# Performance work log

Hardware: AMD Instinct MI355X
Metric: run time of the kernel (lower is better)

## Reference

```python
import jax, jax.numpy as jnp
import numpy as np

N_RES = 8192
N_IN = 128
BATCH = 16
RES_NNZ = int(0.1 * N_RES * N_RES)  # 6710886
IN_NNZ = int(0.1 * N_RES * N_IN)    # 104857
LEAK = 0.9


def spmm_coo(vals, rows, cols, inputs, n_out):
    """COO SpMM: out[b, r] = sum_{n: rows[n]==r} vals[n] * inputs[b, cols[n]].
    Equivalent to (coo_matmat(vals, rows, cols, inputs.T, shape=(n_out, F)).T)."""
    contrib = vals[:, None] * inputs.T[cols]  # [nnz, B]
    return jax.ops.segment_sum(contrib, rows, num_segments=n_out).T  # [B, n_out]


def leaky_erf(z, state, a=LEAK):
    return (1.0 - a) * state + a * jax.scipy.special.erf(z)


def setup_inputs() -> dict:
    key = jax.random.key(0)
    ks = jax.random.split(key, 10)
    return {
        "state": jax.random.normal(ks[0], (BATCH, N_RES), jnp.float32),
        "x": jax.random.normal(ks[1], (BATCH, N_IN), jnp.float32),
        "res_vals": jax.random.normal(ks[2], (RES_NNZ,), jnp.float32),
        "res_rows": jax.random.randint(ks[3], (RES_NNZ,), 0, N_RES, jnp.int32),
        "res_cols": jax.random.randint(ks[4], (RES_NNZ,), 0, N_RES, jnp.int32),
        "res_bias": jax.random.normal(ks[5], (N_RES,), jnp.float32),
        "in_vals": jax.random.normal(ks[6], (IN_NNZ,), jnp.float32),
        "in_rows": jax.random.randint(ks[7], (IN_NNZ,), 0, N_RES, jnp.int32),
        "in_cols": jax.random.randint(ks[8], (IN_NNZ,), 0, N_IN, jnp.int32),
        "in_bias": jax.random.normal(ks[9], (N_RES,), jnp.float32),
    }


def reference(state, x, res_vals, res_rows, res_cols, res_bias,
              in_vals, in_rows, in_cols, in_bias):
    z_res = spmm_coo(res_vals, res_rows, res_cols, state, N_RES) + res_bias
    z_in = spmm_coo(in_vals, in_rows, in_cols, x, N_RES) + in_bias
    return leaky_erf(z_in + z_res, state)
```

## Files before the change

kernel.cpp:

```cpp
#include <hip/hip_runtime.h>
#include <math.h>

#define N_RES 8192
#define N_IN  128
#define BATCH 16
#define LEAK  0.9f

#define NBK    128
#define CAP1B  55296
#define CHUNK1 4096
#define CHUNK2 4096
#define SB2    14
#define TBLK   128


#define OFF_SRCT 0
#define OFF_BCUR (1u << 20)
#define OFF_Z    (2u << 20)
#define OFF_E1   (8u << 20)
#define REQ_A    ((size_t)OFF_E1 + (size_t)NBK * CAP1B * 8)

__global__ __launch_bounds__(256, 4) void pass1_fused(
    const float* __restrict__ state,
    const float* __restrict__ x,
    const float* __restrict__ vres, const int* __restrict__ rres,
    const int* __restrict__ cres, int nres, int nbres,
    const float* __restrict__ vin, const int* __restrict__ rin,
    const int* __restrict__ cin, int nin, int nchunks,
    float* __restrict__ srcT,
    float* __restrict__ z,
    uint2* __restrict__ e1,
    int* __restrict__ bcur) {
  int tid = threadIdx.x;

  if (blockIdx.x >= nchunks) {
    int idx0 = (blockIdx.x - nchunks) * 256 + tid;
    const int stride = TBLK * 256;
    for (int i = idx0; i < N_RES * BATCH; i += stride) {
      int b = i >> 13;
      int r = i & (N_RES - 1);
      srcT[r * BATCH + b] = state[i];
      z[i] = 0.0f;
    }
    for (int i = idx0; i < N_IN * BATCH; i += stride) {
      int b = i >> 7;
      int c = i & (N_IN - 1);
      srcT[(N_RES + c) * BATCH + b] = x[i];
    }
    return;
  }

  const float* vals; const int* rows; const int* cols;
  int nnz, col_off, base;
  if (blockIdx.x < nbres) {
    vals = vres; rows = rres; cols = cres; nnz = nres; col_off = 0;
    base = blockIdx.x * CHUNK1;
  } else {
    vals = vin; rows = rin; cols = cin; nnz = nin; col_off = N_RES;
    base = (blockIdx.x - nbres) * CHUNK1;
  }

  __shared__ uint2 stg[CHUNK1];
  __shared__ int hist[NBK];
  __shared__ int lbase[NBK];
  __shared__ int gbase[NBK];
  __shared__ int wsum[2];
  int wave = tid >> 6, lane = tid & 63;

  if (tid < NBK) hist[tid] = 0;
  __syncthreads();

  int n = nnz - base;
  if (n > CHUNK1) n = CHUNK1;

  uint2 ent[16];
  int lp[16];
  unsigned msk = 0;
#pragma unroll
  for (int g = 0; g < 4; ++g) {
    int i0 = (g * 256 + tid) * 4;
    if (i0 + 3 < n) {
      int4 r4 = *(const int4*)(rows + base + i0);
      int4 c4 = *(const int4*)(cols + base + i0);
      float4 v4 = *(const float4*)(vals + base + i0);
      int rr_[4] = {r4.x, r4.y, r4.z, r4.w};
      int cc_[4] = {c4.x, c4.y, c4.z, c4.w};
      float vv_[4] = {v4.x, v4.y, v4.z, v4.w};
#pragma unroll
      for (int j = 0; j < 4; ++j) {
        int e = g * 4 + j;
        ent[e] = make_uint2(__float_as_uint(vv_[j]),
                            ((unsigned)rr_[j] << 14) |
                                (unsigned)(cc_[j] + col_off));
        msk |= 1u << e;
        lp[e] = atomicAdd(&hist[rr_[j] >> 6], 1);
      }
    } else {
#pragma unroll
      for (int j = 0; j < 4; ++j) {
        int e = g * 4 + j, i = i0 + j;
        if (i < n) {
          int r = rows[base + i];
          int c = cols[base + i] + col_off;
          float v = vals[base + i];
          ent[e] = make_uint2(__float_as_uint(v),
                              ((unsigned)r << 14) | (unsigned)c);
          msk |= 1u << e;
          lp[e] = atomicAdd(&hist[r >> 6], 1);
        }
      }
    }
  }
  __syncthreads();

  int h = 0, v = 0;
  if (tid < NBK) {
    h = hist[tid];
    v = h;
#pragma unroll
    for (int d = 1; d < 64; d <<= 1) {
      int t = __shfl_up(v, d);
      if (lane >= d) v += t;
    }
    if (lane == 63) wsum[wave] = v;
  }
  __syncthreads();
  if (tid < NBK) {
    int off = (wave == 1) ? wsum[0] : 0;
    lbase[tid] = off + v - h;
    gbase[tid] = h ? atomicAdd(&bcur[tid], h) : 0;
  }
  __syncthreads();
#pragma unroll
  for (int e = 0; e < 16; ++e) {
    if (msk & (1u << e)) {
      int b = (int)(ent[e].y >> 20);
      stg[lbase[b] + lp[e]] = ent[e];
    }
  }
  __syncthreads();
  for (int i = tid; i < n; i += 256) {
    uint2 ld = stg[i];
    int b = (int)(ld.y >> 20);
    int p = gbase[b] + (i - lbase[b]);
    if (p < CAP1B) e1[(size_t)b * CAP1B + p] = ld;
  }
}

__global__ __launch_bounds__(512, 8) void pass2_accum(
    const uint2* __restrict__ e1,
    const int* __restrict__ bcur,
    const float* __restrict__ srcT,
    float* __restrict__ z) {
  int bucket = blockIdx.y;
  int ch = blockIdx.x;
  int tid = threadIdx.x;

  int cnt = bcur[bucket];
  if (cnt > CAP1B) cnt = CAP1B;
  int base = ch * CHUNK2;
  if (base >= cnt) return;
  int n = cnt - base;
  if (n > CHUNK2) n = CHUNK2;

  __shared__ uint2 stg[CHUNK2];
  __shared__ int hist[64];
  __shared__ int sbase[65];
  int wave = tid >> 6, lane = tid & 63;
  if (tid < 64) hist[tid] = 0;
  __syncthreads();

  const uint2* __restrict__ src = e1 + (size_t)bucket * CAP1B + base;
  uint2 ent[8];
  int lp[8];
  unsigned msk = 0;
#pragma unroll
  for (int g = 0; g < 4; ++g) {
    int i = (g * 512 + tid) * 2;
    int e = g * 2;
    if (i + 1 < n) {
      uint4 q = *(const uint4*)(src + i);
      ent[e]     = make_uint2(q.x, q.y);
      ent[e + 1] = make_uint2(q.z, q.w);
      msk |= 3u << e;
      lp[e]     = atomicAdd(&hist[(ent[e].y >> 14) & 63u], 1);
      lp[e + 1] = atomicAdd(&hist[(ent[e + 1].y >> 14) & 63u], 1);
    } else if (i < n) {
      ent[e] = src[i];
      msk |= 1u << e;
      lp[e] = atomicAdd(&hist[(ent[e].y >> 14) & 63u], 1);
    }
  }
  __syncthreads();
  if (tid < 64) {
    int hh = hist[tid];
    int vv = hh;
#pragma unroll
    for (int d = 1; d < 64; d <<= 1) {
      int t = __shfl_up(vv, d);
      if (lane >= d) vv += t;
    }
    sbase[tid] = vv - hh;
    if (tid == 63) sbase[64] = vv;
  }
  __syncthreads();
#pragma unroll
  for (int e = 0; e < 8; ++e)
    if (msk & (1u << e))
      stg[sbase[(ent[e].y >> 14) & 63u] + lp[e]] = ent[e];
  __syncthreads();

  int eoff = lane >> 2;
  int bq = lane & 3;
  const float4* __restrict__ s4 = (const float4*)srcT;

  for (int rr = wave * 8; rr < wave * 8 + 8; ++rr) {
    int s0 = sbase[rr], s1 = sbase[rr + 1];
    float4 acc = make_float4(0.f, 0.f, 0.f, 0.f);
    int i0 = s0;
    for (; i0 + 32 <= s1; i0 += 32) {
      uint2 eA = stg[i0 + eoff];
      uint2 eB = stg[i0 + 16 + eoff];
      float4 sA = s4[(int)(eA.y & 16383u) * 4 + bq];
      float4 sB = s4[(int)(eB.y & 16383u) * 4 + bq];
      float vA = __uint_as_float(eA.x);
      float vB = __uint_as_float(eB.x);
      acc.x += vA * sA.x;
      acc.y += vA * sA.y;
      acc.z += vA * sA.z;
      acc.w += vA * sA.w;
      acc.x += vB * sB.x;
      acc.y += vB * sB.y;
      acc.z += vB * sB.z;
      acc.w += vB * sB.w;
    }
    if (i0 + 16 <= s1) {
      uint2 eA = stg[i0 + eoff];
      float4 sA = s4[(int)(eA.y & 16383u) * 4 + bq];
      float vA = __uint_as_float(eA.x);
      acc.x += vA * sA.x;
      acc.y += vA * sA.y;
      acc.z += vA * sA.z;
      acc.w += vA * sA.w;
      i0 += 16;
    }
    if (i0 < s1) {
      int e = i0 + eoff;
      if (e < s1) {
        uint2 eA = stg[e];
        float4 sA = s4[(int)(eA.y & 16383u) * 4 + bq];
        float vA = __uint_as_float(eA.x);
        acc.x += vA * sA.x;
        acc.y += vA * sA.y;
        acc.z += vA * sA.z;
        acc.w += vA * sA.w;
      }
    }
#pragma unroll
    for (int m = 4; m <= 32; m <<= 1) {
      acc.x += __shfl_xor(acc.x, m);
      acc.y += __shfl_xor(acc.y, m);
      acc.z += __shfl_xor(acc.z, m);
      acc.w += __shfl_xor(acc.w, m);
    }
    if (lane < 4) {
      float* zp = z + (size_t)(bucket * 64 + rr) * BATCH + lane * 4;
      unsafeAtomicAdd(zp + 0, acc.x);
      unsafeAtomicAdd(zp + 1, acc.y);
      unsafeAtomicAdd(zp + 2, acc.z);
      unsafeAtomicAdd(zp + 3, acc.w);
    }
  }
}

__global__ __launch_bounds__(256) void finalize_z(
    const float* __restrict__ z, const float* __restrict__ state,
    const float* __restrict__ res_bias, const float* __restrict__ in_bias,
    float* __restrict__ out) {
  int tid = blockIdx.x * 256 + threadIdx.x;
  if (tid >= BATCH * N_RES) return;
  int b = tid >> 13;
  int r = tid & (N_RES - 1);
  float zz = z[r * 16 + b] + res_bias[r] + in_bias[r];
  out[tid] = (1.0f - LEAK) * state[tid] + LEAK * erff(zz);
}

__global__ __launch_bounds__(256) void transpose_nb(
    const float* __restrict__ state, const float* __restrict__ x,
    float* __restrict__ srcT) {
  int tid = blockIdx.x * 256 + threadIdx.x;
  if (tid < N_RES * BATCH) {
    int b = tid >> 13;
    int r = tid & (N_RES - 1);
    srcT[r * BATCH + b] = state[tid];
  }
  if (tid < N_IN * BATCH) {
    int b = tid >> 7;
    int c = tid & (N_IN - 1);
    srcT[(N_RES + c) * BATCH + b] = x[tid];
  }
}

__global__ __launch_bounds__(256) void spmm_atomic(
    const float* __restrict__ vals, const int* __restrict__ rows,
    const int* __restrict__ cols, const float* __restrict__ srcT,
    int col_off, float* __restrict__ zz, int nnz) {
  int i = blockIdx.x * blockDim.x + threadIdx.x;
  if (i >= nnz) return;
  float v = vals[i];
  int r = rows[i];
  int c = cols[i] + col_off;
  const float4* __restrict__ sp = (const float4*)(srcT + c * BATCH);
  float* zr = zz + r * BATCH;
#pragma unroll
  for (int qq = 0; qq < 4; ++qq) {
    float4 s = sp[qq];
    unsafeAtomicAdd(zr + qq * 4 + 0, v * s.x);
    unsafeAtomicAdd(zr + qq * 4 + 1, v * s.y);
    unsafeAtomicAdd(zr + qq * 4 + 2, v * s.z);
    unsafeAtomicAdd(zr + qq * 4 + 3, v * s.w);
  }
}

extern "C" void kernel_launch(void* const* d_in, const int* in_sizes, int n_in,
                              void* d_out, int out_size, void* d_ws, size_t ws_size,
                              hipStream_t stream) {
  const float* state    = (const float*)d_in[0];
  const float* x        = (const float*)d_in[1];
  const float* res_vals = (const float*)d_in[2];
  const int*   res_rows = (const int*)d_in[3];
  const int*   res_cols = (const int*)d_in[4];
  const float* res_bias = (const float*)d_in[5];
  const float* in_vals  = (const float*)d_in[6];
  const int*   in_rows  = (const int*)d_in[7];
  const int*   in_cols  = (const int*)d_in[8];
  const float* in_bias  = (const float*)d_in[9];

  const int res_nnz = in_sizes[2];
  const int in_nnz  = in_sizes[6];

  char* ws = (char*)d_ws;
  float* srcT = (float*)(ws + OFF_SRCT);
  float* z    = (float*)(ws + OFF_Z);
  float* out = (float*)d_out;

  if (ws_size >= REQ_A) {
    int* bcur = (int*)(ws + OFF_BCUR);
    uint2* e1 = (uint2*)(ws + OFF_E1);
    int nbres = (res_nnz + CHUNK1 - 1) / CHUNK1;
    int nbin  = (in_nnz + CHUNK1 - 1) / CHUNK1;
    int nchunks = nbres + nbin;

    hipMemsetAsync(bcur, 0, NBK * sizeof(int), stream);

    pass1_fused<<<nchunks + TBLK, 256, 0, stream>>>(
        state, x, res_vals, res_rows, res_cols, res_nnz, nbres,
        in_vals, in_rows, in_cols, in_nnz, nchunks, srcT, z, e1, bcur);

    pass2_accum<<<dim3(SB2, NBK), 512, 0, stream>>>(e1, bcur, srcT, z);

    finalize_z<<<512, 256, 0, stream>>>(z, state, res_bias, in_bias, out);
  } else {
    hipMemsetAsync(z, 0, N_RES * BATCH * sizeof(float), stream);
    transpose_nb<<<512, 256, 0, stream>>>(state, x, srcT);
    spmm_atomic<<<(res_nnz + 255) / 256, 256, 0, stream>>>(
        res_vals, res_rows, res_cols, srcT, 0, z, res_nnz);
    spmm_atomic<<<(in_nnz + 255) / 256, 256, 0, stream>>>(
        in_vals, in_rows, in_cols, srcT, N_RES, z, in_nnz);
    finalize_z<<<512, 256, 0, stream>>>(z, state, res_bias, in_bias, out);
  }
}
```

Baseline: 212.4 us.

## Double pass1 chunk/block size and unroll pass2 gather loop with dual accumulators

Pass1 now runs 512-thread blocks that each bin an 8192-entry chunk, halving the block count and the global bucket atomics per entry. Pass2's inner gather loop is unrolled to four gathers per iteration into two accumulators, with a scheduling barrier so all loads issue before the FMAs, raising memory-level parallelism. The larger staging buffer raises LDS use per block and may lower occupancy. Code that still assumes 256 threads could misbehave.

```diff
diff --git a/kernel.cpp b/kernel.cpp
--- a/kernel.cpp
+++ b/kernel.cpp
@@ -8,7 +8,7 @@
 
 #define NBK    128
 #define CAP1B  55296
-#define CHUNK1 4096
+#define CHUNK1 8192
 #define CHUNK2 4096
 #define SB2    14
 #define TBLK   128
@@ -20,7 +20,7 @@
 #define OFF_E1   (8u << 20)
 #define REQ_A    ((size_t)OFF_E1 + (size_t)NBK * CAP1B * 8)
 
-__global__ __launch_bounds__(256, 4) void pass1_fused(
+__global__ __launch_bounds__(512, 4) void pass1_fused(
     const float* __restrict__ state,
     const float* __restrict__ x,
     const float* __restrict__ vres, const int* __restrict__ rres,
@@ -34,8 +34,8 @@
   int tid = threadIdx.x;
 
   if (blockIdx.x >= nchunks) {
-    int idx0 = (blockIdx.x - nchunks) * 256 + tid;
-    const int stride = TBLK * 256;
+    int idx0 = (blockIdx.x - nchunks) * 512 + tid;
+    const int stride = TBLK * 512;
     for (int i = idx0; i < N_RES * BATCH; i += stride) {
       int b = i >> 13;
       int r = i & (N_RES - 1);
@@ -78,7 +78,7 @@
   unsigned msk = 0;
 #pragma unroll
   for (int g = 0; g < 4; ++g) {
-    int i0 = (g * 256 + tid) * 4;
+    int i0 = (g * 512 + tid) * 4;
     if (i0 + 3 < n) {
       int4 r4 = *(const int4*)(rows + base + i0);
       int4 c4 = *(const int4*)(cols + base + i0);
@@ -139,7 +139,7 @@
     }
   }
   __syncthreads();
-  for (int i = tid; i < n; i += 256) {
+  for (int i = tid; i < n; i += 512) {
     uint2 ld = stg[i];
     int b = (int)(ld.y >> 20);
     int p = gbase[b] + (i - lbase[b]);
@@ -216,32 +216,52 @@
 
   for (int rr = wave * 8; rr < wave * 8 + 8; ++rr) {
     int s0 = sbase[rr], s1 = sbase[rr + 1];
-    float4 acc = make_float4(0.f, 0.f, 0.f, 0.f);
+    float4 accA = make_float4(0.f, 0.f, 0.f, 0.f);
+    float4 accB = make_float4(0.f, 0.f, 0.f, 0.f);
     int i0 = s0;
-    for (; i0 + 32 <= s1; i0 += 32) {
+    for (; i0 + 64 <= s1; i0 += 64) {
+      uint2 eA = stg[i0 + eoff];
+      uint2 eB = stg[i0 + 16 + eoff];
+      uint2 eC = stg[i0 + 32 + eoff];
+      uint2 eD = stg[i0 + 48 + eoff];
+      float4 sA = s4[(int)(eA.y & 16383u) * 4 + bq];
+      float4 sB = s4[(int)(eB.y & 16383u) * 4 + bq];
+      float4 sC = s4[(int)(eC.y & 16383u) * 4 + bq];
+      float4 sD = s4[(int)(eD.y & 16383u) * 4 + bq];
+      __builtin_amdgcn_sched_barrier(0);
+      float vA = __uint_as_float(eA.x);
+      float vB = __uint_as_float(eB.x);
+      float vC = __uint_as_float(eC.x);
+      float vD = __uint_as_float(eD.x);
+      accA.x += vA * sA.x; accA.y += vA * sA.y;
+      accA.z += vA * sA.z; accA.w += vA * sA.w;
+      accB.x += vB * sB.x; accB.y += vB * sB.y;
+      accB.z += vB * sB.z; accB.w += vB * sB.w;
+      accA.x += vC * sC.x; accA.y += vC * sC.y;
+      accA.z += vC * sC.z; accA.w += vC * sC.w;
+      accB.x += vD * sD.x; accB.y += vD * sD.y;
+      accB.z += vD * sD.z; accB.w += vD * sD.w;
+    }
+    if (i0 + 32 <= s1) {
       uint2 eA = stg[i0 + eoff];
       uint2 eB = stg[i0 + 16 + eoff];
       float4 sA = s4[(int)(eA.y & 16383u) * 4 + bq];
       float4 sB = s4[(int)(eB.y & 16383u) * 4 + bq];
+      __builtin_amdgcn_sched_barrier(0);
       float vA = __uint_as_float(eA.x);
       float vB = __uint_as_float(eB.x);
-      acc.x += vA * sA.x;
-      acc.y += vA * sA.y;
-      acc.z += vA * sA.z;
-      acc.w += vA * sA.w;
-      acc.x += vB * sB.x;
-      acc.y += vB * sB.y;
-      acc.z += vB * sB.z;
-      acc.w += vB * sB.w;
+      accA.x += vA * sA.x; accA.y += vA * sA.y;
+      accA.z += vA * sA.z; accA.w += vA * sA.w;
+      accB.x += vB * sB.x; accB.y += vB * sB.y;
+      accB.z += vB * sB.z; accB.w += vB * sB.w;
+      i0 += 32;
     }
     if (i0 + 16 <= s1) {
       uint2 eA = stg[i0 + eoff];
       float4 sA = s4[(int)(eA.y & 16383u) * 4 + bq];
       float vA = __uint_as_float(eA.x);
-      acc.x += vA * sA.x;
-      acc.y += vA * sA.y;
-      acc.z += vA * sA.z;
-      acc.w += vA * sA.w;
+      accA.x += vA * sA.x; accA.y += vA * sA.y;
+      accA.z += vA * sA.z; accA.w += vA * sA.w;
       i0 += 16;
     }
     if (i0 < s1) {
@@ -250,12 +270,12 @@
         uint2 eA = stg[e];
         float4 sA = s4[(int)(eA.y & 16383u) * 4 + bq];
         float vA = __uint_as_float(eA.x);
-        acc.x += vA * sA.x;
-        acc.y += vA * sA.y;
-        acc.z += vA * sA.z;
-        acc.w += vA * sA.w;
+        accA.x += vA * sA.x; accA.y += vA * sA.y;
+        accA.z += vA * sA.z; accA.w += vA * sA.w;
       }
     }
+    float4 acc = make_float4(accA.x + accB.x, accA.y + accB.y,
+                             accA.z + accB.z, accA.w + accB.w);
 #pragma unroll
     for (int m = 4; m <= 32; m <<= 1) {
       acc.x += __shfl_xor(acc.x, m);
@@ -353,7 +373,7 @@
 
     hipMemsetAsync(bcur, 0, NBK * sizeof(int), stream);
 
-    pass1_fused<<<nchunks + TBLK, 256, 0, stream>>>(
+    pass1_fused<<<nchunks + TBLK, 512, 0, stream>>>(
         state, x, res_vals, res_rows, res_cols, res_nnz, nbres,
         in_vals, in_rows, in_cols, in_nnz, nchunks, srcT, z, e1, bcur);
 
```

Result: faster. 202.0 us (-4.9%).
